# Performance work log

Hardware: AMD Instinct MI355X
Metric: run time of the kernel (lower is better)

## Reference

```python
import jax, jax.numpy as jnp
import numpy as np

N, E, T, B = 10000, 80000, 240000, 32
HF, EMB = 256, 64
EDGE_BINS, ANG_BINS = 80, 40
N_CONV = 12  # 4 alignn layers x 2 EGGC + 4 gcn EGGC


def layernorm(x, scale, bias):
    m = x.mean(-1, keepdims=True)
    v = ((x - m) ** 2).mean(-1, keepdims=True)
    return (x - m) / jnp.sqrt(v + 1e-5) * scale + bias


def mlp_layer(x, W, b, ln):
    # Linear -> LayerNorm -> SiLU
    return jax.nn.silu(layernorm(x @ W + b, ln[0], ln[1]))


def rbf(x, vmin, vmax, bins):
    centers = jnp.linspace(vmin, vmax, bins)
    gamma = 0.5 / ((vmax - vmin) / bins) ** 2
    return jnp.exp(-gamma * (x[..., None] - centers) ** 2)


def eggc(W, b, ln_s, ln_b, src, dst, h, e, n_nodes):
    """Edge-gated graph conv. W:[5,F,F] b:[5,F] order: src_gate,dst_gate,edge_gate,src_update,dst_update.
    ln_s/ln_b:[2,F] order: edges, nodes."""
    e_src = h @ W[0] + b[0]
    e_dst = h @ W[1] + b[1]
    sigma = jax.nn.sigmoid(e_src[src] + e_dst[dst] + e @ W[2] + b[2])  # [n_edges, F]
    e_out = layernorm(sigma * e, ln_s[0], ln_b[0])
    Bh = h @ W[4] + b[4]  # dst_update
    sum_sh = jax.ops.segment_sum(Bh[src] * sigma, dst, num_segments=n_nodes)
    sum_s = jax.ops.segment_sum(sigma, dst, num_segments=n_nodes)
    h_out = h @ W[3] + b[3] + sum_sh / (sum_s + 1e-8)  # src_update + gated mean
    return layernorm(h_out, ln_s[1], ln_b[1]), e_out


def setup_inputs() -> dict:
    key = jax.random.key(0)
    ks = jax.random.split(key, 24)
    rn = lambda k, shp: (jax.random.normal(k, shp, dtype=jnp.float32) * 0.05)
    ln_init = lambda f: jnp.stack([jnp.ones((f,), jnp.float32), jnp.zeros((f,), jnp.float32)])
    inp = {
        'atom_features': jax.random.normal(ks[0], (N, 92), dtype=jnp.float32),
        'bondlength': jax.random.uniform(ks[1], (E,), dtype=jnp.float32) * 8.0,
        'angle_h': jax.random.uniform(ks[2], (T,), dtype=jnp.float32) * 2.0 - 1.0,
        'src': jax.random.randint(ks[3], (E,), 0, N, dtype=jnp.int32),
        'dst': jax.random.randint(ks[4], (E,), 0, N, dtype=jnp.int32),
        'lg_src': jax.random.randint(ks[5], (T,), 0, E, dtype=jnp.int32),
        'lg_dst': jax.random.randint(ks[6], (T,), 0, E, dtype=jnp.int32),
        'graph_ids': jnp.sort(jax.random.randint(ks[7], (N,), 0, B)).astype(jnp.int32),
        'atom_W': rn(ks[8], (92, HF)), 'atom_b': jnp.zeros((HF,), jnp.float32), 'atom_ln': ln_init(HF),
        'edge_W1': rn(ks[9], (EDGE_BINS, EMB)), 'edge_b1': jnp.zeros((EMB,), jnp.float32), 'edge_ln1': ln_init(EMB),
        'edge_W2': rn(ks[10], (EMB, HF)), 'edge_b2': jnp.zeros((HF,), jnp.float32), 'edge_ln2': ln_init(HF),
        'ang_W1': rn(ks[11], (ANG_BINS, EMB)), 'ang_b1': jnp.zeros((EMB,), jnp.float32), 'ang_ln1': ln_init(EMB),
        'ang_W2': rn(ks[12], (EMB, HF)), 'ang_b2': jnp.zeros((HF,), jnp.float32), 'ang_ln2': ln_init(HF),
        'conv_W': rn(ks[13], (N_CONV, 5, HF, HF)),
        'conv_b': jnp.zeros((N_CONV, 5, HF), jnp.float32),
        'conv_ln_s': jnp.ones((N_CONV, 2, HF), jnp.float32),
        'conv_ln_b': jnp.zeros((N_CONV, 2, HF), jnp.float32),
    }
    return inp


def reference(atom_features, bondlength, angle_h, src, dst, lg_src, lg_dst, graph_ids,
              atom_W, atom_b, atom_ln, edge_W1, edge_b1, edge_ln1, edge_W2, edge_b2, edge_ln2,
              ang_W1, ang_b1, ang_ln1, ang_W2, ang_b2, ang_ln2,
              conv_W, conv_b, conv_ln_s, conv_ln_b):
    n_nodes = atom_features.shape[0]
    n_edges = bondlength.shape[0]
    # embeddings
    z = mlp_layer(mlp_layer(rbf(angle_h, -1.0, 1.0, ANG_BINS), ang_W1, ang_b1, ang_ln1), ang_W2, ang_b2, ang_ln2)
    x = mlp_layer(atom_features, atom_W, atom_b, atom_ln)
    y = mlp_layer(mlp_layer(rbf(bondlength, 0.0, 8.0, EDGE_BINS), edge_W1, edge_b1, edge_ln1), edge_W2, edge_b2, edge_ln2)
    # 4 ALIGNN layers: edge_update on line graph, then node_update on graph
    for i in range(4):
        j = 2 * i
        y, z = eggc(conv_W[j], conv_b[j], conv_ln_s[j], conv_ln_b[j], lg_src, lg_dst, y, z, n_edges)
        j = 2 * i + 1
        x, y = eggc(conv_W[j], conv_b[j], conv_ln_s[j], conv_ln_b[j], src, dst, x, y, n_nodes)
    # 4 GCN layers
    for i in range(4):
        j = 8 + i
        x, y = eggc(conv_W[j], conv_b[j], conv_ln_s[j], conv_ln_b[j], src, dst, x, y, n_nodes)
    # AvgPooling readout per graph
    sums = jax.ops.segment_sum(x, graph_ids, num_segments=B)
    counts = jax.ops.segment_sum(jnp.ones((n_nodes,), x.dtype), graph_ids, num_segments=B)
    return sums / jnp.maximum(counts, 1.0)[:, None]
```

## Files before the change

kernel.cpp:

```cpp
#include <hip/hip_runtime.h>
#include <hip/hip_bf16.h>

typedef unsigned short u16;
typedef unsigned int u32;
typedef __attribute__((ext_vector_type(8))) short short8;
typedef __attribute__((ext_vector_type(4))) float f32x4;

__device__ __forceinline__ float bf2f(u16 u) { return __uint_as_float(((u32)u) << 16); }
__device__ __forceinline__ u16 f2bf(float f) {
  u32 x = __float_as_uint(f);
  return (u16)((x + 0x7FFFu + ((x >> 16) & 1u)) >> 16);
}
__device__ __forceinline__ void up4(uint2 r, float* o) {
  o[0] = bf2f((u16)(r.x & 0xFFFF)); o[1] = bf2f((u16)(r.x >> 16));
  o[2] = bf2f((u16)(r.y & 0xFFFF)); o[3] = bf2f((u16)(r.y >> 16));
}
__device__ __forceinline__ uint2 pk4(const float* o) {
  uint2 r;
  r.x = (u32)f2bf(o[0]) | ((u32)f2bf(o[1]) << 16);
  r.y = (u32)f2bf(o[2]) | ((u32)f2bf(o[3]) << 16);
  return r;
}
__device__ __forceinline__ void up8(uint4 r, float* o) {
  o[0] = bf2f((u16)(r.x & 0xFFFF)); o[1] = bf2f((u16)(r.x >> 16));
  o[2] = bf2f((u16)(r.y & 0xFFFF)); o[3] = bf2f((u16)(r.y >> 16));
  o[4] = bf2f((u16)(r.z & 0xFFFF)); o[5] = bf2f((u16)(r.z >> 16));
  o[6] = bf2f((u16)(r.w & 0xFFFF)); o[7] = bf2f((u16)(r.w >> 16));
}
__device__ __forceinline__ uint4 pk8(const float* o) {
  uint4 r;
  r.x = (u32)f2bf(o[0]) | ((u32)f2bf(o[1]) << 16);
  r.y = (u32)f2bf(o[2]) | ((u32)f2bf(o[3]) << 16);
  r.z = (u32)f2bf(o[4]) | ((u32)f2bf(o[5]) << 16);
  r.w = (u32)f2bf(o[6]) | ((u32)f2bf(o[7]) << 16);
  return r;
}
__device__ __forceinline__ float wsum64(float v) {
#pragma unroll
  for (int o = 32; o > 0; o >>= 1) v += __shfl_xor(v, o, 64);
  return v;
}
__device__ __forceinline__ float wsum16(float v) {
#pragma unroll
  for (int o = 8; o > 0; o >>= 1) v += __shfl_xor(v, o, 64);
  return v;
}
__device__ __forceinline__ float sigm(float x) { return 1.0f / (1.0f + __expf(-x)); }

__global__ __launch_bounds__(256) void fill_kernel(float* __restrict__ out, int n, float v) {
  int i = blockIdx.x * 256 + threadIdx.x;
  if (i < n) out[i] = v;
}

__global__ __launch_bounds__(256) void wtrans(const float* __restrict__ in,
                                              u16* __restrict__ out, int R, int Ccols) {
  __shared__ float t[64][65];
  const float* ip = in + (size_t)blockIdx.z * R * Ccols;
  u16* op = out + (size_t)blockIdx.z * R * Ccols;
  int kb = blockIdx.x * 64, nb = blockIdx.y * 64;
  int lr = threadIdx.x >> 4, lc = (threadIdx.x & 15) * 4;
#pragma unroll
  for (int p = 0; p < 4; ++p) {
    int k = lr + p * 16;
    float4 v = *(const float4*)(ip + (size_t)(kb + k) * Ccols + nb + lc);
    t[k][lc + 0] = v.x; t[k][lc + 1] = v.y; t[k][lc + 2] = v.z; t[k][lc + 3] = v.w;
  }
  __syncthreads();
#pragma unroll
  for (int p = 0; p < 4; ++p) {
    int n = lr + p * 16;
    uint2 pk;
    pk.x = (u32)f2bf(t[lc + 0][n]) | ((u32)f2bf(t[lc + 1][n]) << 16);
    pk.y = (u32)f2bf(t[lc + 2][n]) | ((u32)f2bf(t[lc + 3][n]) << 16);
    *(uint2*)(op + (size_t)(nb + n) * R + kb + lc) = pk;
  }
}

__global__ __launch_bounds__(256) void csr_hist(const int* __restrict__ dst,
                                                int* __restrict__ hist, int ne) {
  int e = blockIdx.x * 256 + threadIdx.x;
  if (e < ne) atomicAdd(&hist[dst[e]], 1);
}
__global__ __launch_bounds__(1024) void scan1(const int* __restrict__ in,
                                              int* __restrict__ out1, int* __restrict__ bsum, int n) {
  __shared__ int s[1024];
  int i = blockIdx.x * 1024 + threadIdx.x;
  int v = (i < n) ? in[i] : 0;
  s[threadIdx.x] = v; __syncthreads();
  for (int off = 1; off < 1024; off <<= 1) {
    int t = (threadIdx.x >= (u32)off) ? s[threadIdx.x - off] : 0;
    __syncthreads();
    s[threadIdx.x] += t;
    __syncthreads();
  }
  if (i < n) out1[i] = s[threadIdx.x];
  if (threadIdx.x == 1023) bsum[blockIdx.x] = s[1023];
}
__global__ __launch_bounds__(128) void scan2(int* __restrict__ bsum, int nb) {
  __shared__ int s[128];
  int v = (threadIdx.x < (u32)nb) ? bsum[threadIdx.x] : 0;
  s[threadIdx.x] = v; __syncthreads();
  for (int off = 1; off < 128; off <<= 1) {
    int t = (threadIdx.x >= (u32)off) ? s[threadIdx.x - off] : 0;
    __syncthreads();
    s[threadIdx.x] += t;
    __syncthreads();
  }
  if (threadIdx.x < (u32)nb) bsum[threadIdx.x] = threadIdx.x ? s[threadIdx.x - 1] : 0;
}
__global__ __launch_bounds__(256) void scan3(int* __restrict__ offs,
                                             const int* __restrict__ bsum, int n) {
  int i = blockIdx.x * 256 + threadIdx.x;
  if (i == 0) offs[0] = 0;
  if (i < n) offs[1 + i] += bsum[i >> 10];
}
__global__ __launch_bounds__(256) void csr_scatter(const int* __restrict__ dst,
                                                   int* __restrict__ cursor,
                                                   const int* __restrict__ offs,
                                                   int* __restrict__ eid, int ne) {
  int e = blockIdx.x * 256 + threadIdx.x;
  if (e < ne) {
    int d = dst[e];
    int p = offs[d] + atomicAdd(&cursor[d], 1);
    eid[p] = e;
  }
}
__global__ __launch_bounds__(256) void inv_perm(const int* __restrict__ eid,
                                                int* __restrict__ pos, int n) {
  int i = blockIdx.x * 256 + threadIdx.x;
  if (i < n) pos[eid[i]] = i;
}
__global__ __launch_bounds__(256) void remap_k(const int* __restrict__ idx,
                                               const int* __restrict__ map,
                                               int* __restrict__ out, int n) {
  int i = blockIdx.x * 256 + threadIdx.x;
  if (i < n) out[i] = map[idx[i]];
}
__global__ __launch_bounds__(256) void compose_src(const int* __restrict__ eid,
                                                   const int* __restrict__ srcv,
                                                   const int* __restrict__ map,
                                                   int* __restrict__ out, int n) {
  int i = blockIdx.x * 256 + threadIdx.x;
  if (i < n) {
    int s = srcv[eid[i]];
    out[i] = map ? map[s] : s;
  }
}

__global__ __launch_bounds__(256) void embed_s1(
    const float* __restrict__ xin, const float* __restrict__ W1,
    const float* __restrict__ b1, const float* __restrict__ ln1,
    u16* __restrict__ t1, int rows, int bins, float vmin, float vmax,
    const int* __restrict__ perm) {
  int row = (blockIdx.x * 256 + threadIdx.x) >> 6;
  if (row >= rows) return;
  int lane = threadIdx.x & 63;
  float xv = xin[row];
  float rng = vmax - vmin;
  float step = rng / (float)(bins - 1);
  float gamma = 0.5f * ((float)bins / rng) * ((float)bins / rng);
  float rb = 0.f, rb2 = 0.f;
  if (lane < bins) {
    float d = xv - (vmin + lane * step);
    rb = __expf(-gamma * d * d);
  }
  if (bins > 64 && lane < bins - 64) {
    float d = xv - (vmin + (lane + 64) * step);
    rb2 = __expf(-gamma * d * d);
  }
  float u = b1[lane];
  int k1 = bins < 64 ? bins : 64;
  for (int k = 0; k < k1; ++k) {
    float rv = __shfl(rb, k, 64);
    u = fmaf(rv, W1[k * 64 + lane], u);
  }
  for (int k = 64; k < bins; ++k) {
    float rv = __shfl(rb2, k - 64, 64);
    u = fmaf(rv, W1[k * 64 + lane], u);
  }
  float s = wsum64(u), s2 = wsum64(u * u);
  float m = s * (1.f / 64.f), var = s2 * (1.f / 64.f) - m * m;
  float t = (u - m) * rsqrtf(var + 1e-5f) * ln1[lane] + ln1[64 + lane];
  int orow = perm ? perm[row] : row;
  t1[(size_t)orow * 64 + lane] = f2bf(t * sigm(t));
}

__global__ __launch_bounds__(256) void ln_silu(u16* __restrict__ buf,
                                               const float* __restrict__ ln, int rows) {
  int row = (blockIdx.x * 256 + threadIdx.x) >> 6;
  if (row >= rows) return;
  int lane = threadIdx.x & 63;
  int f = lane * 4;
  float v[4];
  up4(*(const uint2*)(buf + (size_t)row * 256 + f), v);
  float s = wsum64(v[0] + v[1] + v[2] + v[3]);
  float s2 = wsum64(v[0] * v[0] + v[1] * v[1] + v[2] * v[2] + v[3] * v[3]);
  float m = s * (1.f / 256.f);
  float rs = rsqrtf(s2 * (1.f / 256.f) - m * m + 1e-5f);
  float o[4];
#pragma unroll
  for (int k = 0; k < 4; ++k) {
    float t = (v[k] - m) * rs * ln[f + k] + ln[256 + f + k];
    o[k] = t * sigm(t);
  }
  *(uint2*)(buf + (size_t)row * 256 + f) = pk4(o);
}

__global__ __launch_bounds__(256) void atom_embed_kernel(
    const float* __restrict__ af, const float* __restrict__ W,
    const float* __restrict__ b, const float* __restrict__ ln,
    u16* __restrict__ out, int rows) {
  int row = blockIdx.x;
  if (row >= rows) return;
  __shared__ float a_s[92];
  __shared__ float red[8];
  int tid = threadIdx.x;
  if (tid < 92) a_s[tid] = af[(size_t)row * 92 + tid];
  __syncthreads();
  float v = b[tid];
#pragma unroll 4
  for (int k = 0; k < 92; ++k) v = fmaf(a_s[k], W[k * 256 + tid], v);
  float s = wsum64(v), s2 = wsum64(v * v);
  int lane = tid & 63, wid = tid >> 6;
  if (lane == 0) { red[wid] = s; red[4 + wid] = s2; }
  __syncthreads();
  s = red[0] + red[1] + red[2] + red[3];
  s2 = red[4] + red[5] + red[6] + red[7];
  float m = s * (1.f / 256.f), var = s2 * (1.f / 256.f) - m * m;
  float t = (v - m) * rsqrtf(var + 1e-5f) * ln[tid] + ln[256 + tid];
  out[(size_t)row * 256 + tid] = f2bf(t * sigm(t));
}

__global__ __launch_bounds__(256) void mfma_gemm(
    const u16* __restrict__ A, const u16* __restrict__ Wt,
    const float* __restrict__ bias, u16* __restrict__ C,
    int M, int K, int ldc, u32 smap) {
  int bm = blockIdx.x * 128;
  if (bm >= M) return;
  int bn = blockIdx.y * 128;
  int slab = (smap >> ((bn >> 8) * 8)) & 0xFF;
  const u16* Wp = Wt + (size_t)slab * 256 * K + (size_t)(bn & 255) * K;
  const float* bp = bias + slab * 256 + (bn & 255);
  int tid = threadIdx.x;
  int w = tid >> 6, lane = tid & 63;
  int q = lane >> 4, r = lane & 15;
  int m0 = (w & 1) * 64;
  int n0 = (w >> 1) * 64;
  const u16* aptr[4];
#pragma unroll
  for (int mi = 0; mi < 4; ++mi) {
    int m = bm + m0 + mi * 16 + r;
    m = m < M - 1 ? m : M - 1;
    aptr[mi] = A + (size_t)m * K + q * 8;
  }
  const u16* wptr[4];
#pragma unroll
  for (int ni = 0; ni < 4; ++ni)
    wptr[ni] = Wp + (size_t)(n0 + ni * 16 + r) * K + q * 8;
  f32x4 acc[4][4] = {};
  for (int kb = 0; kb < K; kb += 32) {
    short8 bfr[4], afr[4];
#pragma unroll
    for (int mi = 0; mi < 4; ++mi) bfr[mi] = *(const short8*)(aptr[mi] + kb);
#pragma unroll
    for (int ni = 0; ni < 4; ++ni) afr[ni] = *(const short8*)(wptr[ni] + kb);
#pragma unroll
    for (int mi = 0; mi < 4; ++mi)
#pragma unroll
      for (int ni = 0; ni < 4; ++ni)
        acc[mi][ni] = __builtin_amdgcn_mfma_f32_16x16x32_bf16(afr[ni], bfr[mi],
                                                              acc[mi][ni], 0, 0, 0);
  }
#pragma unroll
  for (int mi = 0; mi < 4; ++mi) {
    int m = bm + m0 + mi * 16 + r;
    if (m < M) {
#pragma unroll
      for (int ni = 0; ni < 4; ++ni) {
        int n = n0 + ni * 16 + q * 4;
        float4 bv = *(const float4*)(bp + n);
        uint2 o;
        o.x = (u32)f2bf(acc[mi][ni].x + bv.x) | ((u32)f2bf(acc[mi][ni].y + bv.y) << 16);
        o.y = (u32)f2bf(acc[mi][ni].z + bv.z) | ((u32)f2bf(acc[mi][ni].w + bv.w) << 16);
        *(uint2*)(C + (size_t)m * ldc + bn + n) = o;
      }
    }
  }
}

__global__ __launch_bounds__(512) void mega_line(
    u16* __restrict__ h, u16* __restrict__ e, const u16* __restrict__ G0Bh,
    const u16* __restrict__ Wt13, const float* __restrict__ b13,
    const u16* __restrict__ Wt2, const float* __restrict__ b2v,
    const int* __restrict__ src_perm, const int* __restrict__ offs,
    const float* __restrict__ lnS, const float* __restrict__ lnB, int nn) {
  __shared__ u16 g1ah[16][520];
  __shared__ u16 pe[64][264];
  __shared__ int oloc[17];
  int tid = threadIdx.x;
  int w = tid >> 6, lane = tid & 63;
  int q = lane >> 4, r = lane & 15;
  int v0 = blockIdx.x * 16;
  if (tid < 17) { int v = v0 + tid; oloc[tid] = offs[v < nn ? v : nn]; }
  {
    int mrow = v0 + r; if (mrow > nn - 1) mrow = nn - 1;
    const u16* arow = h + (size_t)mrow * 256 + q * 8;
    f32x4 acc[4] = {};
    for (int kb = 0; kb < 256; kb += 32) {
      short8 af = *(const short8*)(arow + kb);
#pragma unroll
      for (int t = 0; t < 4; ++t) {
        int ng = (4 * w + t) * 16 + r;
        const u16* wrow = Wt13 + (size_t)(ng >> 8) * 2 * 65536 +
                          (size_t)(ng & 255) * 256 + q * 8;
        short8 wf = *(const short8*)(wrow + kb);
        acc[t] = __builtin_amdgcn_mfma_f32_16x16x32_bf16(wf, af, acc[t], 0, 0, 0);
      }
    }
#pragma unroll
    for (int t = 0; t < 4; ++t) {
      int nb = (4 * w + t) * 16 + q * 4;
      const float* bp = b13 + (nb >> 8) * 2 * 256 + (nb & 255);
      float o[4] = {acc[t].x + bp[0], acc[t].y + bp[1], acc[t].z + bp[2], acc[t].w + bp[3]};
      *(uint2*)&g1ah[r][nb] = pk4(o);
    }
  }
  __syncthreads();
  int gl = lane & 15;
  int qg = lane >> 4;
  int dd = w * 2 + (qg >> 1);
  int half = qg & 1;
  int vv = v0 + dd;
  int fa = gl * 8;
  int fB = 128 + gl * 8;
  int r0 = oloc[0], r1 = oloc[16];
  int d0 = oloc[dd], d1 = oloc[dd + 1];
  float lwe[16], lbe[16];
#pragma unroll
  for (int k = 0; k < 8; ++k) {
    lwe[k] = lnS[fa + k];     lbe[k] = lnB[fa + k];
    lwe[8 + k] = lnS[fB + k]; lbe[8 + k] = lnB[fB + k];
  }
  uint4 g1p0 = *(const uint4*)&g1ah[dd][fa];
  uint4 g1p1 = *(const uint4*)&g1ah[dd][fB];
  float ssh[16] = {}, ssm[16] = {};

  for (int ec = r0; ec < r1; ec += 64) {
    {
      const u16* w0p = Wt2 + (size_t)((2 * w) * 16 + r) * 256 + q * 8;
      const u16* w1p = Wt2 + (size_t)((2 * w + 1) * 16 + r) * 256 + q * 8;
      f32x4 acc[4][2] = {};
      for (int kb = 0; kb < 256; kb += 32) {
        short8 wf0 = *(const short8*)(w0p + kb);
        short8 wf1 = *(const short8*)(w1p + kb);
#pragma unroll
        for (int mt = 0; mt < 4; ++mt) {
          int erow = ec + mt * 16 + r;
          if (erow > r1 - 1) erow = r1 - 1;
          short8 af = *(const short8*)(e + (size_t)erow * 256 + kb + q * 8);
          acc[mt][0] = __builtin_amdgcn_mfma_f32_16x16x32_bf16(wf0, af, acc[mt][0], 0, 0, 0);
          acc[mt][1] = __builtin_amdgcn_mfma_f32_16x16x32_bf16(wf1, af, acc[mt][1], 0, 0, 0);
        }
      }
#pragma unroll
      for (int mt = 0; mt < 4; ++mt)
#pragma unroll
        for (int nt = 0; nt < 2; ++nt) {
          int nb = (2 * w + nt) * 16 + q * 4;
          float o[4] = {acc[mt][nt].x + b2v[nb], acc[mt][nt].y + b2v[nb + 1],
                        acc[mt][nt].z + b2v[nb + 2], acc[mt][nt].w + b2v[nb + 3]};
          *(uint2*)&pe[mt * 16 + r][nb] = pk4(o);
        }
    }
    __syncthreads();
    {
      int ce = ec + 64 < r1 ? ec + 64 : r1;
      int i0 = d0 > ec ? d0 : ec;
      int i1 = d1 < ce ? d1 : ce;
      int is = i0 + half;
      if (is < i1) {
        int sv = src_perm[is];
        uint4 pg0a = *(const uint4*)(G0Bh + (size_t)sv * 512 + fa);
        uint4 pg0b = *(const uint4*)(G0Bh + (size_t)sv * 512 + fB);
        uint4 pbha = *(const uint4*)(G0Bh + (size_t)sv * 512 + 256 + fa);
        uint4 pbhb = *(const uint4*)(G0Bh + (size_t)sv * 512 + 256 + fB);
        for (int i = is; i < i1; i += 2) {
          uint4 cg0a = pg0a, cg0b = pg0b, cbha = pbha, cbhb = pbhb;
          if (i + 2 < i1) {
            int sv2 = src_perm[i + 2];
            pg0a = *(const uint4*)(G0Bh + (size_t)sv2 * 512 + fa);
            pg0b = *(const uint4*)(G0Bh + (size_t)sv2 * 512 + fB);
            pbha = *(const uint4*)(G0Bh + (size_t)sv2 * 512 + 256 + fa);
            pbhb = *(const uint4*)(G0Bh + (size_t)sv2 * 512 + 256 + fB);
          }
          float g0[16], bh[16], pv[16], ev[16], g1v[16];
          up8(cg0a, g0); up8(cg0b, g0 + 8);
          up8(cbha, bh); up8(cbhb, bh + 8);
          up8(*(const uint4*)&pe[i - ec][fa], pv);
          up8(*(const uint4*)&pe[i - ec][fB], pv + 8);
          up8(*(const uint4*)(e + (size_t)i * 256 + fa), ev);
          up8(*(const uint4*)(e + (size_t)i * 256 + fB), ev + 8);
          up8(g1p0, g1v); up8(g1p1, g1v + 8);
          float t[16];
          float ssum = 0.f, s2sum = 0.f;
#pragma unroll
          for (int k = 0; k < 16; ++k) {
            float sg = sigm(g0[k] + g1v[k] + pv[k]);
            t[k] = sg * ev[k];
            ssh[k] = fmaf(bh[k], sg, ssh[k]);
            ssm[k] += sg;
            ssum += t[k]; s2sum += t[k] * t[k];
          }
          float s1 = wsum16(ssum), s2 = wsum16(s2sum);
          float mn = s1 * (1.f / 256.f);
          float rs = rsqrtf(s2 * (1.f / 256.f) - mn * mn + 1e-5f);
          float o[16];
#pragma unroll
          for (int k = 0; k < 16; ++k) o[k] = (t[k] - mn) * rs * lwe[k] + lbe[k];
          *(uint4*)(e + (size_t)i * 256 + fa) = pk8(o);
          *(uint4*)(e + (size_t)i * 256 + fB) = pk8(o + 8);
        }
      }
    }
    __syncthreads();
  }
#pragma unroll
  for (int k = 0; k < 16; ++k) {
    ssh[k] += __shfl_xor(ssh[k], 16, 64);
    ssm[k] += __shfl_xor(ssm[k], 16, 64);
  }
  if (half == 0 && vv < nn) {
    float ah[16], tt[16];
    up8(*(const uint4*)&g1ah[dd][256 + fa], ah);
    up8(*(const uint4*)&g1ah[dd][256 + fB], ah + 8);
    float ssum = 0.f, s2sum = 0.f;
#pragma unroll
    for (int k = 0; k < 16; ++k) {
      tt[k] = ah[k] + ssh[k] / (ssm[k] + 1e-8f);
      ssum += tt[k]; s2sum += tt[k] * tt[k];
    }
    float s1 = wsum16(ssum), s2 = wsum16(s2sum);
    float mn = s1 * (1.f / 256.f);
    float rs = rsqrtf(s2 * (1.f / 256.f) - mn * mn + 1e-5f);
    float o[16];
#pragma unroll
    for (int k = 0; k < 8; ++k) {
      o[k] = (tt[k] - mn) * rs * lnS[256 + fa + k] + lnB[256 + fa + k];
      o[8 + k] = (tt[8 + k] - mn) * rs * lnS[256 + fB + k] + lnB[256 + fB + k];
    }
    *(uint4*)(h + (size_t)vv * 256 + fa) = pk8(o);
    *(uint4*)(h + (size_t)vv * 256 + fB) = pk8(o + 8);
  }
}

__global__ __launch_bounds__(512) void mega_atom(
    u16* __restrict__ h, u16* __restrict__ e, const u16* __restrict__ GAll,
    const u16* __restrict__ Wt2, const float* __restrict__ b2v,
    const int* __restrict__ src_perm, const int* __restrict__ offs,
    const float* __restrict__ lnS, const float* __restrict__ lnB, int nn) {
  __shared__ u16 pe[64][264];
  __shared__ int oloc[17];
  int tid = threadIdx.x;
  int w = tid >> 6, lane = tid & 63;
  int q = lane >> 4, r = lane & 15;
  int v0 = blockIdx.x * 16;
  if (tid < 17) { int v = v0 + tid; oloc[tid] = offs[v < nn ? v : nn]; }
  __syncthreads();
  int gl = lane & 15;
  int qg = lane >> 4;
  int dd = w * 2 + (qg >> 1);
  int half = qg & 1;
  int vv = v0 + dd;
  int fa = gl * 8;
  int fB = 128 + gl * 8;
  int r0 = oloc[0], r1 = oloc[16];
  int d0 = oloc[dd], d1 = oloc[dd + 1];
  float lwe[16], lbe[16];
#pragma unroll
  for (int k = 0; k < 8; ++k) {
    lwe[k] = lnS[fa + k];     lbe[k] = lnB[fa + k];
    lwe[8 + k] = lnS[fB + k]; lbe[8 + k] = lnB[fB + k];
  }
  int vc = vv < nn ? vv : nn - 1;
  uint4 g1p0 = *(const uint4*)(GAll + (size_t)vc * 1024 + 256 + fa);
  uint4 g1p1 = *(const uint4*)(GAll + (size_t)vc * 1024 + 256 + fB);
  float ssh[16] = {}, ssm[16] = {};

  for (int ec = r0; ec < r1; ec += 64) {
    {
      const u16* w0p = Wt2 + (size_t)((2 * w) * 16 + r) * 256 + q * 8;
      const u16* w1p = Wt2 + (size_t)((2 * w + 1) * 16 + r) * 256 + q * 8;
      f32x4 acc[4][2] = {};
      for (int kb = 0; kb < 256; kb += 32) {
        short8 wf0 = *(const short8*)(w0p + kb);
        short8 wf1 = *(const short8*)(w1p + kb);
#pragma unroll
        for (int mt = 0; mt < 4; ++mt) {
          int erow = ec + mt * 16 + r;
          if (erow > r1 - 1) erow = r1 - 1;
          short8 af = *(const short8*)(e + (size_t)erow * 256 + kb + q * 8);
          acc[mt][0] = __builtin_amdgcn_mfma_f32_16x16x32_bf16(wf0, af, acc[mt][0], 0, 0, 0);
          acc[mt][1] = __builtin_amdgcn_mfma_f32_16x16x32_bf16(wf1, af, acc[mt][1], 0, 0, 0);
        }
      }
#pragma unroll
      for (int mt = 0; mt < 4; ++mt)
#pragma unroll
        for (int nt = 0; nt < 2; ++nt) {
          int nb = (2 * w + nt) * 16 + q * 4;
          float o[4] = {acc[mt][nt].x + b2v[nb], acc[mt][nt].y + b2v[nb + 1],
                        acc[mt][nt].z + b2v[nb + 2], acc[mt][nt].w + b2v[nb + 3]};
          *(uint2*)&pe[mt * 16 + r][nb] = pk4(o);
        }
    }
    __syncthreads();
    {
      int ce = ec + 64 < r1 ? ec + 64 : r1;
      int i0 = d0 > ec ? d0 : ec;
      int i1 = d1 < ce ? d1 : ce;
      int is = i0 + half;
      if (is < i1) {
        int sv = src_perm[is];
        uint4 pg0a = *(const uint4*)(GAll + (size_t)sv * 1024 + fa);
        uint4 pg0b = *(const uint4*)(GAll + (size_t)sv * 1024 + fB);
        uint4 pbha = *(const uint4*)(GAll + (size_t)sv * 1024 + 768 + fa);
        uint4 pbhb = *(const uint4*)(GAll + (size_t)sv * 1024 + 768 + fB);
        for (int i = is; i < i1; i += 2) {
          uint4 cg0a = pg0a, cg0b = pg0b, cbha = pbha, cbhb = pbhb;
          if (i + 2 < i1) {
            int sv2 = src_perm[i + 2];
            pg0a = *(const uint4*)(GAll + (size_t)sv2 * 1024 + fa);
            pg0b = *(const uint4*)(GAll + (size_t)sv2 * 1024 + fB);
            pbha = *(const uint4*)(GAll + (size_t)sv2 * 1024 + 768 + fa);
            pbhb = *(const uint4*)(GAll + (size_t)sv2 * 1024 + 768 + fB);
          }
          float g0[16], bh[16], pv[16], ev[16], g1v[16];
          up8(cg0a, g0); up8(cg0b, g0 + 8);
          up8(cbha, bh); up8(cbhb, bh + 8);
          up8(*(const uint4*)&pe[i - ec][fa], pv);
          up8(*(const uint4*)&pe[i - ec][fB], pv + 8);
          up8(*(const uint4*)(e + (size_t)i * 256 + fa), ev);
          up8(*(const uint4*)(e + (size_t)i * 256 + fB), ev + 8);
          up8(g1p0, g1v); up8(g1p1, g1v + 8);
          float t[16];
          float ssum = 0.f, s2sum = 0.f;
#pragma unroll
          for (int k = 0; k < 16; ++k) {
            float sg = sigm(g0[k] + g1v[k] + pv[k]);
            t[k] = sg * ev[k];
            ssh[k] = fmaf(bh[k], sg, ssh[k]);
            ssm[k] += sg;
            ssum += t[k]; s2sum += t[k] * t[k];
          }
          float s1 = wsum16(ssum), s2 = wsum16(s2sum);
          float mn = s1 * (1.f / 256.f);
          float rs = rsqrtf(s2 * (1.f / 256.f) - mn * mn + 1e-5f);
          float o[16];
#pragma unroll
          for (int k = 0; k < 16; ++k) o[k] = (t[k] - mn) * rs * lwe[k] + lbe[k];
          *(uint4*)(e + (size_t)i * 256 + fa) = pk8(o);
          *(uint4*)(e + (size_t)i * 256 + fB) = pk8(o + 8);
        }
      }
    }
    __syncthreads();
  }
#pragma unroll
  for (int k = 0; k < 16; ++k) {
    ssh[k] += __shfl_xor(ssh[k], 16, 64);
    ssm[k] += __shfl_xor(ssm[k], 16, 64);
  }
  if (half == 0 && vv < nn) {
    float ah[16], tt[16];
    up8(*(const uint4*)(GAll + (size_t)vv * 1024 + 512 + fa), ah);
    up8(*(const uint4*)(GAll + (size_t)vv * 1024 + 512 + fB), ah + 8);
    float ssum = 0.f, s2sum = 0.f;
#pragma unroll
    for (int k = 0; k < 16; ++k) {
      tt[k] = ah[k] + ssh[k] / (ssm[k] + 1e-8f);
      ssum += tt[k]; s2sum += tt[k] * tt[k];
    }
    float s1 = wsum16(ssum), s2 = wsum16(s2sum);
    float mn = s1 * (1.f / 256.f);
    float rs = rsqrtf(s2 * (1.f / 256.f) - mn * mn + 1e-5f);
    float o[16];
#pragma unroll
    for (int k = 0; k < 8; ++k) {
      o[k] = (tt[k] - mn) * rs * lnS[256 + fa + k] + lnB[256 + fa + k];
      o[8 + k] = (tt[8 + k] - mn) * rs * lnS[256 + fB + k] + lnB[256 + fB + k];
    }
    *(uint4*)(h + (size_t)vv * 256 + fa) = pk8(o);
    *(uint4*)(h + (size_t)vv * 256 + fB) = pk8(o + 8);
  }
}

__global__ __launch_bounds__(256) void pool_acc(
    const u16* __restrict__ x, const int* __restrict__ gid,
    float* __restrict__ out, float* __restrict__ cnt, int n) {
  int v = (blockIdx.x * 256 + threadIdx.x) >> 6;
  if (v >= n) return;
  int lane = threadIdx.x & 63;
  int f = lane * 4;
  int g = gid[v];
  float xv[4];
  up4(*(const uint2*)(x + (size_t)v * 256 + f), xv);
  float* p = out + (size_t)g * 256 + f;
  unsafeAtomicAdd(p + 0, xv[0]);
  unsafeAtomicAdd(p + 1, xv[1]);
  unsafeAtomicAdd(p + 2, xv[2]);
  unsafeAtomicAdd(p + 3, xv[3]);
  if (lane == 0) unsafeAtomicAdd(cnt + g, 1.0f);
}
__global__ __launch_bounds__(256) void pool_div(float* __restrict__ out,
                                                const float* __restrict__ cnt, int n) {
  int i = blockIdx.x * blockDim.x + threadIdx.x;
  if (i < n) out[i] /= fmaxf(cnt[i >> 8], 1.0f);
}

extern "C" void kernel_launch(void* const* d_in, const int* in_sizes, int n_in,
                              void* d_out, int out_size, void* d_ws, size_t ws_size,
                              hipStream_t stream) {
  const float* atom_features = (const float*)d_in[0];
  const float* bondlength    = (const float*)d_in[1];
  const float* angle_h       = (const float*)d_in[2];
  const int*   src           = (const int*)d_in[3];
  const int*   dst           = (const int*)d_in[4];
  const int*   lg_src        = (const int*)d_in[5];
  const int*   lg_dst        = (const int*)d_in[6];
  const int*   gid           = (const int*)d_in[7];
  const float* atom_W  = (const float*)d_in[8];
  const float* atom_b  = (const float*)d_in[9];
  const float* atom_ln = (const float*)d_in[10];
  const float* edge_W1 = (const float*)d_in[11];
  const float* edge_b1 = (const float*)d_in[12];
  const float* edge_ln1= (const float*)d_in[13];
  const float* edge_W2 = (const float*)d_in[14];
  const float* edge_b2 = (const float*)d_in[15];
  const float* edge_ln2= (const float*)d_in[16];
  const float* ang_W1  = (const float*)d_in[17];
  const float* ang_b1  = (const float*)d_in[18];
  const float* ang_ln1 = (const float*)d_in[19];
  const float* ang_W2  = (const float*)d_in[20];
  const float* ang_b2  = (const float*)d_in[21];
  const float* ang_ln2 = (const float*)d_in[22];
  const float* conv_W  = (const float*)d_in[23];
  const float* conv_b  = (const float*)d_in[24];
  const float* conv_lns= (const float*)d_in[25];
  const float* conv_lnb= (const float*)d_in[26];

  int N = in_sizes[0] / 92;
  int E = in_sizes[1];
  int T = in_sizes[2];

  char* ws = (char*)d_ws;
  size_t o = 0;
  auto alloc = [&](size_t bytes) { size_t r = o; o = (o + bytes + 255) & ~(size_t)255; return r; };
  u16* z     = (u16*)(ws + alloc((size_t)T * 512));
  u16* y     = (u16*)(ws + alloc((size_t)E * 512));
  u16* x     = (u16*)(ws + alloc((size_t)N * 512));
  int* offsL = (int*)(ws + alloc((size_t)(E + 1) * 4));
  int* offsA = (int*)(ws + alloc((size_t)(N + 1) * 4));
  int* spL   = (int*)(ws + alloc((size_t)T * 4));
  int* spA   = (int*)(ws + alloc((size_t)E * 4));
  int* pA    = (int*)(ws + alloc((size_t)E * 4));
  int* pL    = (int*)(ws + alloc((size_t)T * 4));
  int* eidL  = (int*)(ws + alloc((size_t)T * 4));
  int* eidA  = (int*)(ws + alloc((size_t)E * 4));
  int* ldSt  = (int*)(ws + alloc((size_t)T * 4));
  int* tmp   = (int*)(ws + alloc((size_t)(E > N ? E : N) * 4));
  int* bsum  = (int*)(ws + alloc(1024));
  float* cnt = (float*)(ws + alloc(1024));
  u16* WtAll = (u16*)(ws + alloc((size_t)12 * 5 * 65536 * 2));
  u16* WtAng = (u16*)(ws + alloc((size_t)16384 * 2));
  u16* WtEdg = (u16*)(ws + alloc((size_t)16384 * 2));
  size_t scratch_base = o;
  size_t need = scratch_base + (size_t)E * 1024;
  {
    size_t embed_need = scratch_base + ((size_t)T + E) * 128;
    if (embed_need > need) need = embed_need;
  }
  if (ws_size < need) {
    fill_kernel<<<(out_size + 255) / 256, 256, 0, stream>>>(
        (float*)d_out, out_size, (float)(ws_size >> 20));
    return;
  }

  wtrans<<<dim3(4, 4, 60), 256, 0, stream>>>(conv_W, WtAll, 256, 256);
  wtrans<<<dim3(1, 4, 1), 256, 0, stream>>>(ang_W2, WtAng, 64, 256);
  wtrans<<<dim3(1, 4, 1), 256, 0, stream>>>(edge_W2, WtEdg, 64, 256);

  auto build_csr = [&](const int* dvec, int ne_, int nn_, int* offs_, int* eid_) {
    hipMemsetAsync(tmp, 0, (size_t)nn_ * 4, stream);
    csr_hist<<<(ne_ + 255) / 256, 256, 0, stream>>>(dvec, tmp, ne_);
    int nb = (nn_ + 1023) / 1024;
    scan1<<<nb, 1024, 0, stream>>>(tmp, offs_ + 1, bsum, nn_);
    scan2<<<1, 128, 0, stream>>>(bsum, nb);
    scan3<<<(nn_ + 255) / 256, 256, 0, stream>>>(offs_, bsum, nn_);
    hipMemsetAsync(tmp, 0, (size_t)nn_ * 4, stream);
    csr_scatter<<<(ne_ + 255) / 256, 256, 0, stream>>>(dvec, tmp, offs_, eid_, ne_);
  };
  build_csr(dst, E, N, offsA, eidA);
  inv_perm<<<(E + 255) / 256, 256, 0, stream>>>(eidA, pA, E);
  compose_src<<<(E + 255) / 256, 256, 0, stream>>>(eidA, src, nullptr, spA, E);
  remap_k<<<(T + 255) / 256, 256, 0, stream>>>(lg_dst, pA, ldSt, T);
  build_csr(ldSt, T, E, offsL, eidL);
  inv_perm<<<(T + 255) / 256, 256, 0, stream>>>(eidL, pL, T);
  compose_src<<<(T + 255) / 256, 256, 0, stream>>>(eidL, lg_src, pA, spL, T);

  u16* t1T = (u16*)(ws + scratch_base);
  u16* t1E = t1T + (size_t)T * 64;
  embed_s1<<<(T + 3) / 4, 256, 0, stream>>>(angle_h, ang_W1, ang_b1, ang_ln1,
                                            t1T, T, 40, -1.f, 1.f, pL);
  embed_s1<<<(E + 3) / 4, 256, 0, stream>>>(bondlength, edge_W1, edge_b1, edge_ln1,
                                            t1E, E, 80, 0.f, 8.f, pA);
  mfma_gemm<<<dim3((T + 127) / 128, 2), 256, 0, stream>>>(
      t1T, WtAng, ang_b2, z, T, 64, 256, 0u);
  mfma_gemm<<<dim3((E + 127) / 128, 2), 256, 0, stream>>>(
      t1E, WtEdg, edge_b2, y, E, 64, 256, 0u);
  ln_silu<<<(T + 3) / 4, 256, 0, stream>>>(z, ang_ln2, T);
  ln_silu<<<(E + 3) / 4, 256, 0, stream>>>(y, edge_ln2, E);
  atom_embed_kernel<<<N, 256, 0, stream>>>(atom_features, atom_W, atom_b, atom_ln, x, N);

  for (int l = 0; l < 12; ++l) {
    const u16* WtL  = WtAll + (size_t)l * 5 * 65536;
    const float* bl = conv_b + (size_t)l * 5 * 256;
    const float* lnS = conv_lns + (size_t)l * 512;
    const float* lnB = conv_lnb + (size_t)l * 512;
    bool line = (l < 8) && ((l & 1) == 0);
    if (line) {
      u16* G0Bh = (u16*)(ws + scratch_base);
      mfma_gemm<<<dim3((E + 127) / 128, 4), 256, 0, stream>>>(
          y, WtL, bl, G0Bh, E, 256, 512, 0u | (4u << 8));
      mega_line<<<(E + 15) / 16, 512, 0, stream>>>(
          y, z, G0Bh, WtL + 65536, bl + 256, WtL + 2 * 65536, bl + 2 * 256,
          spL, offsL, lnS, lnB, E);
    } else {
      u16* GAll = (u16*)(ws + scratch_base);
      mfma_gemm<<<dim3((N + 127) / 128, 8), 256, 0, stream>>>(
          x, WtL, bl, GAll, N, 256, 1024, 0u | (1u << 8) | (3u << 16) | (4u << 24));
      mega_atom<<<(N + 15) / 16, 512, 0, stream>>>(
          x, y, GAll, WtL + 2 * 65536, bl + 2 * 256,
          spA, offsA, lnS, lnB, N);
    }
  }

  hipMemsetAsync(d_out, 0, (size_t)out_size * sizeof(float), stream);
  hipMemsetAsync(cnt, 0, 256 * sizeof(float), stream);
  pool_acc<<<(N + 3) / 4, 256, 0, stream>>>(x, gid, (float*)d_out, cnt, N);
  pool_div<<<(out_size + 255) / 256, 256, 0, stream>>>((float*)d_out, cnt, out_size);
}
```

Baseline: 5.230 ms.

## Split edge-gate GEMM out of mega_atom into standalone MFMA GEMM

The fused in-block edge-gate GEMM (e @ W[2]) is removed from mega_atom and computed by a separate mfma_gemm over all edges into a global Pe buffer. mega_atom then just reads the precomputed Pe rows, drops shared memory and block syncs, and uses 256-thread blocks covering 8 nodes. This aims to remove the per-block chunked GEMM with redundant W reloads and barrier stalls, at the cost of an extra kernel launch and a round trip of E×256 bf16 through global memory.

Result: faster. 4.677 ms, median of 3 (-10.6%).

```diff
diff --git a/kernel.cpp b/kernel.cpp
--- a/kernel.cpp
+++ b/kernel.cpp
@@ -453,18 +453,16 @@
   }
 }
 
-__global__ __launch_bounds__(512) void mega_atom(
+__global__ __launch_bounds__(256) void mega_atom(
     u16* __restrict__ h, u16* __restrict__ e, const u16* __restrict__ GAll,
-    const u16* __restrict__ Wt2, const float* __restrict__ b2v,
+    const u16* __restrict__ Pe,
     const int* __restrict__ src_perm, const int* __restrict__ offs,
     const float* __restrict__ lnS, const float* __restrict__ lnB, int nn) {
-  __shared__ u16 pe[64][264];
-  __shared__ int oloc[17];
+  __shared__ int oloc[9];
   int tid = threadIdx.x;
   int w = tid >> 6, lane = tid & 63;
-  int q = lane >> 4, r = lane & 15;
-  int v0 = blockIdx.x * 16;
-  if (tid < 17) { int v = v0 + tid; oloc[tid] = offs[v < nn ? v : nn]; }
+  int v0 = blockIdx.x * 8;
+  if (tid < 9) { int v = v0 + tid; oloc[tid] = offs[v < nn ? v : nn]; }
   __syncthreads();
   int gl = lane & 15;
   int qg = lane >> 4;
@@ -473,7 +471,6 @@
   int vv = v0 + dd;
   int fa = gl * 8;
   int fB = 128 + gl * 8;
-  int r0 = oloc[0], r1 = oloc[16];
   int d0 = oloc[dd], d1 = oloc[dd + 1];
   float lwe[16], lbe[16];
 #pragma unroll
@@ -486,84 +483,49 @@
   uint4 g1p1 = *(const uint4*)(GAll + (size_t)vc * 1024 + 256 + fB);
   float ssh[16] = {}, ssm[16] = {};
 
-  for (int ec = r0; ec < r1; ec += 64) {
-    {
-      const u16* w0p = Wt2 + (size_t)((2 * w) * 16 + r) * 256 + q * 8;
-      const u16* w1p = Wt2 + (size_t)((2 * w + 1) * 16 + r) * 256 + q * 8;
-      f32x4 acc[4][2] = {};
-      for (int kb = 0; kb < 256; kb += 32) {
-        short8 wf0 = *(const short8*)(w0p + kb);
-        short8 wf1 = *(const short8*)(w1p + kb);
-#pragma unroll
-        for (int mt = 0; mt < 4; ++mt) {
-          int erow = ec + mt * 16 + r;
-          if (erow > r1 - 1) erow = r1 - 1;
-          short8 af = *(const short8*)(e + (size_t)erow * 256 + kb + q * 8);
-          acc[mt][0] = __builtin_amdgcn_mfma_f32_16x16x32_bf16(wf0, af, acc[mt][0], 0, 0, 0);
-          acc[mt][1] = __builtin_amdgcn_mfma_f32_16x16x32_bf16(wf1, af, acc[mt][1], 0, 0, 0);
-        }
+  int is = d0 + half;
+  if (is < d1) {
+    int sv = src_perm[is];
+    uint4 pg0a = *(const uint4*)(GAll + (size_t)sv * 1024 + fa);
+    uint4 pg0b = *(const uint4*)(GAll + (size_t)sv * 1024 + fB);
+    uint4 pbha = *(const uint4*)(GAll + (size_t)sv * 1024 + 768 + fa);
+    uint4 pbhb = *(const uint4*)(GAll + (size_t)sv * 1024 + 768 + fB);
+    for (int i = is; i < d1; i += 2) {
+      uint4 cg0a = pg0a, cg0b = pg0b, cbha = pbha, cbhb = pbhb;
+      if (i + 2 < d1) {
+        int sv2 = src_perm[i + 2];
+        pg0a = *(const uint4*)(GAll + (size_t)sv2 * 1024 + fa);
+        pg0b = *(const uint4*)(GAll + (size_t)sv2 * 1024 + fB);
+        pbha = *(const uint4*)(GAll + (size_t)sv2 * 1024 + 768 + fa);
+        pbhb = *(const uint4*)(GAll + (size_t)sv2 * 1024 + 768 + fB);
       }
-#pragma unroll
-      for (int mt = 0; mt < 4; ++mt)
-#pragma unroll
-        for (int nt = 0; nt < 2; ++nt) {
-          int nb = (2 * w + nt) * 16 + q * 4;
-          float o[4] = {acc[mt][nt].x + b2v[nb], acc[mt][nt].y + b2v[nb + 1],
-                        acc[mt][nt].z + b2v[nb + 2], acc[mt][nt].w + b2v[nb + 3]};
-          *(uint2*)&pe[mt * 16 + r][nb] = pk4(o);
-        }
-    }
-    __syncthreads();
-    {
-      int ce = ec + 64 < r1 ? ec + 64 : r1;
-      int i0 = d0 > ec ? d0 : ec;
-      int i1 = d1 < ce ? d1 : ce;
-      int is = i0 + half;
-      if (is < i1) {
-        int sv = src_perm[is];
-        uint4 pg0a = *(const uint4*)(GAll + (size_t)sv * 1024 + fa);
-        uint4 pg0b = *(const uint4*)(GAll + (size_t)sv * 1024 + fB);
-        uint4 pbha = *(const uint4*)(GAll + (size_t)sv * 1024 + 768 + fa);
-        uint4 pbhb = *(const uint4*)(GAll + (size_t)sv * 1024 + 768 + fB);
-        for (int i = is; i < i1; i += 2) {
-          uint4 cg0a = pg0a, cg0b = pg0b, cbha = pbha, cbhb = pbhb;
-          if (i + 2 < i1) {
-            int sv2 = src_perm[i + 2];
-            pg0a = *(const uint4*)(GAll + (size_t)sv2 * 1024 + fa);
-            pg0b = *(const uint4*)(GAll + (size_t)sv2 * 1024 + fB);
-            pbha = *(const uint4*)(GAll + (size_t)sv2 * 1024 + 768 + fa);
-            pbhb = *(const uint4*)(GAll + (size_t)sv2 * 1024 + 768 + fB);
-          }
-          float g0[16], bh[16], pv[16], ev[16], g1v[16];
-          up8(cg0a, g0); up8(cg0b, g0 + 8);
-          up8(cbha, bh); up8(cbhb, bh + 8);
-          up8(*(const uint4*)&pe[i - ec][fa], pv);
-          up8(*(const uint4*)&pe[i - ec][fB], pv + 8);
-          up8(*(const uint4*)(e + (size_t)i * 256 + fa), ev);
-          up8(*(const uint4*)(e + (size_t)i * 256 + fB), ev + 8);
-          up8(g1p0, g1v); up8(g1p1, g1v + 8);
-          float t[16];
-          float ssum = 0.f, s2sum = 0.f;
-#pragma unroll
-          for (int k = 0; k < 16; ++k) {
-            float sg = sigm(g0[k] + g1v[k] + pv[k]);
-            t[k] = sg * ev[k];
-            ssh[k] = fmaf(bh[k], sg, ssh[k]);
-            ssm[k] += sg;
-            ssum += t[k]; s2sum += t[k] * t[k];
-          }
-          float s1 = wsum16(ssum), s2 = wsum16(s2sum);
-          float mn = s1 * (1.f / 256.f);
-          float rs = rsqrtf(s2 * (1.f / 256.f) - mn * mn + 1e-5f);
-          float o[16];
-#pragma unroll
-          for (int k = 0; k < 16; ++k) o[k] = (t[k] - mn) * rs * lwe[k] + lbe[k];
-          *(uint4*)(e + (size_t)i * 256 + fa) = pk8(o);
-          *(uint4*)(e + (size_t)i * 256 + fB) = pk8(o + 8);
-        }
+      float g0[16], bh[16], pv[16], ev[16], g1v[16];
+      up8(cg0a, g0); up8(cg0b, g0 + 8);
+      up8(cbha, bh); up8(cbhb, bh + 8);
+      up8(*(const uint4*)(Pe + (size_t)i * 256 + fa), pv);
+      up8(*(const uint4*)(Pe + (size_t)i * 256 + fB), pv + 8);
+      up8(*(const uint4*)(e + (size_t)i * 256 + fa), ev);
+      up8(*(const uint4*)(e + (size_t)i * 256 + fB), ev + 8);
+      up8(g1p0, g1v); up8(g1p1, g1v + 8);
+      float t[16];
+      float ssum = 0.f, s2sum = 0.f;
+#pragma unroll
+      for (int k = 0; k < 16; ++k) {
+        float sg = sigm(g0[k] + g1v[k] + pv[k]);
+        t[k] = sg * ev[k];
+        ssh[k] = fmaf(bh[k], sg, ssh[k]);
+        ssm[k] += sg;
+        ssum += t[k]; s2sum += t[k] * t[k];
       }
-    }
-    __syncthreads();
+      float s1 = wsum16(ssum), s2 = wsum16(s2sum);
+      float mn = s1 * (1.f / 256.f);
+      float rs = rsqrtf(s2 * (1.f / 256.f) - mn * mn + 1e-5f);
+      float o[16];
+#pragma unroll
+      for (int k = 0; k < 16; ++k) o[k] = (t[k] - mn) * rs * lwe[k] + lbe[k];
+      *(uint4*)(e + (size_t)i * 256 + fa) = pk8(o);
+      *(uint4*)(e + (size_t)i * 256 + fB) = pk8(o + 8);
+    }
   }
 #pragma unroll
   for (int k = 0; k < 16; ++k) {
@@ -676,6 +638,8 @@
   size_t scratch_base = o;
   size_t need = scratch_base + (size_t)E * 1024;
   {
+    size_t atom_need = scratch_base + (size_t)N * 2048 + (size_t)E * 512;
+    if (atom_need > need) need = atom_need;
     size_t embed_need = scratch_base + ((size_t)T + E) * 128;
     if (embed_need > need) need = embed_need;
   }
@@ -736,11 +700,13 @@
           spL, offsL, lnS, lnB, E);
     } else {
       u16* GAll = (u16*)(ws + scratch_base);
+      u16* PeA  = GAll + (size_t)N * 1024;
       mfma_gemm<<<dim3((N + 127) / 128, 8), 256, 0, stream>>>(
           x, WtL, bl, GAll, N, 256, 1024, 0u | (1u << 8) | (3u << 16) | (4u << 24));
-      mega_atom<<<(N + 15) / 16, 512, 0, stream>>>(
-          x, y, GAll, WtL + 2 * 65536, bl + 2 * 256,
-          spA, offsA, lnS, lnB, N);
+      mfma_gemm<<<dim3((E + 127) / 128, 2), 256, 0, stream>>>(
+          y, WtL + 2 * 65536, bl + 2 * 256, PeA, E, 256, 256, 0u);
+      mega_atom<<<(N + 7) / 8, 256, 0, stream>>>(
+          x, y, GAll, PeA, spA, offsA, lnS, lnB, N);
     }
   }
 
```
